# Performance work log

Hardware: AMD Instinct MI355X
Metric: run time of the kernel (lower is better)

## Reference

```python
import jax, jax.numpy as jnp
import numpy as np

VOCAB, EMB, HID, NCLS = 50257, 48, 128, 2000
B, S = 512, 1024


def setup_inputs() -> dict:
    key = jax.random.key(0)
    ks = jax.random.split(key, 8)
    x = jax.random.randint(ks[0], (B, S), 0, VOCAB)
    emb_table = jax.random.normal(ks[1], (VOCAB, EMB), dtype=jnp.float32)
    emb_table = emb_table.at[0].set(0.0)  # padding_idx=0
    k_ih = 1.0 / np.sqrt(HID)
    w_ih = jax.random.uniform(ks[2], (4 * HID, EMB), minval=-k_ih, maxval=k_ih, dtype=jnp.float32)
    w_hh = jax.random.uniform(ks[3], (4 * HID, HID), minval=-k_ih, maxval=k_ih, dtype=jnp.float32)
    b_ih = jax.random.uniform(ks[4], (4 * HID,), minval=-k_ih, maxval=k_ih, dtype=jnp.float32)
    b_hh = jax.random.uniform(ks[5], (4 * HID,), minval=-k_ih, maxval=k_ih, dtype=jnp.float32)
    k_fc = 1.0 / np.sqrt(HID)
    w_fc = jax.random.uniform(ks[6], (NCLS, HID), minval=-k_fc, maxval=k_fc, dtype=jnp.float32)
    b_fc = jax.random.uniform(ks[7], (NCLS,), minval=-k_fc, maxval=k_fc, dtype=jnp.float32)
    return {"x": x, "emb_table": emb_table, "w_ih": w_ih, "w_hh": w_hh,
            "b_ih": b_ih, "b_hh": b_hh, "w_fc": w_fc, "b_fc": b_fc}


def _lstm_last_hidden(e, w_ih, w_hh, b_ih, b_hh):
    # e: [B, S, E]. Precompute input contributions for all timesteps (one big GEMM).
    xg = jnp.einsum('bse,ge->bsg', e, w_ih) + b_ih + b_hh  # [B, S, 4H]
    xg = jnp.transpose(xg, (1, 0, 2))                      # [S, B, 4H]
    Bn = e.shape[0]
    h0 = jnp.zeros((Bn, HID), e.dtype)
    c0 = jnp.zeros((Bn, HID), e.dtype)

    def step(carry, xg_t):
        h, c = carry
        g = xg_t + h @ w_hh.T                              # [B, 4H]
        i, f, gg, o = jnp.split(g, 4, axis=-1)             # PyTorch gate order i,f,g,o
        i = jax.nn.sigmoid(i)
        f = jax.nn.sigmoid(f)
        gg = jnp.tanh(gg)
        o = jax.nn.sigmoid(o)
        c = f * c + i * gg
        h = o * jnp.tanh(c)
        return (h, c), None

    (h_n, _), _ = jax.lax.scan(step, (h0, c0), xg)
    return h_n


def reference(x, emb_table, w_ih, w_hh, b_ih, b_hh, w_fc, b_fc):
    e = emb_table[x]                                       # [B, S, E] gather
    h_n = _lstm_last_hidden(e, w_ih, w_hh, b_ih, b_hh)     # [B, H]
    return h_n @ w_fc.T + b_fc                             # [B, NCLS]
```

## Files before the change

### kernel.cpp

```cpp
#include <hip/hip_runtime.h>

#define DI __device__ __forceinline__

typedef unsigned int uint;
typedef unsigned short ushort;
typedef _Float16 half2t __attribute__((ext_vector_type(2)));

#define VOCAB 50257
#define NEMB 48
#define HID 128
#define G4 512
#define NCLS 2000
#define BATCH 512
#define SEQ 1024

#if __has_builtin(__builtin_amdgcn_fdot2)
DI float fdot2(half2t a, half2t b, float c) { return __builtin_amdgcn_fdot2(a, b, c, false); }
#else
DI float fdot2(half2t a, half2t b, float c) { return c + (float)a.x * (float)b.x + (float)a.y * (float)b.y; }
#endif

DI float sigm(float x) {
  return __builtin_amdgcn_rcpf(1.0f + __builtin_amdgcn_exp2f(-1.4426950408889634f * x));
}
DI float tanhfast(float x) {
  return 1.0f - 2.0f * __builtin_amdgcn_rcpf(__builtin_amdgcn_exp2f(2.8853900817779268f * x) + 1.0f);
}

DI void barrier_lds_only() {
  asm volatile("s_waitcnt lgkmcnt(0)" ::: "memory");
  __builtin_amdgcn_s_barrier();
  asm volatile("" ::: "memory");
}

#define VROWS 32
__global__ __launch_bounds__(512) void build_P(
    const float* __restrict__ emb, const float* __restrict__ w_ih,
    const float* __restrict__ b_ih, const float* __restrict__ b_hh,
    _Float16* __restrict__ P)
{
  __shared__ __align__(16) float eL[VROWS][NEMB];
  const int tid = threadIdx.x;
  const int v0 = blockIdx.x * VROWS;
  int nrows = VOCAB - v0; if (nrows > VROWS) nrows = VROWS;

  for (int f = tid; f < nrows * NEMB; f += 512)
    eL[f / NEMB][f % NEMB] = emb[(size_t)v0 * NEMB + f];

  float w[NEMB];
  {
    const float* wr = w_ih + (size_t)tid * NEMB;
#pragma unroll
    for (int k = 0; k < NEMB; k++) w[k] = wr[k];
  }
  float bias = b_ih[tid] + b_hh[tid];
  __syncthreads();

  for (int v = 0; v < nrows; v++) {
    const float4* e4 = (const float4*)&eL[v][0];
    float a = bias;
#pragma unroll
    for (int k = 0; k < NEMB / 4; k++) {
      float4 e = e4[k];
      a += w[4 * k] * e.x + w[4 * k + 1] * e.y + w[4 * k + 2] * e.z + w[4 * k + 3] * e.w;
    }
    P[(size_t)(v0 + v) * G4 + tid] = (_Float16)a;
  }
}

template<bool USE_P>
__global__ __launch_bounds__(512, 4) void lstm_scan(
    const int* __restrict__ x, const float* __restrict__ emb,
    const float* __restrict__ w_ih, const float* __restrict__ w_hh,
    const float* __restrict__ b_ih, const float* __restrict__ b_hh,
    const _Float16* __restrict__ P, float* __restrict__ hout)
{
  __shared__ int tokL[SEQ];
  __shared__ __align__(16) _Float16 h16[HID];
  __shared__ float g2h[2][G4];
  __shared__ __align__(8) half2t e16[2][NEMB / 2];

  const int tid = threadIdx.x;
  const int b = blockIdx.x;
  const int col = tid & 255;
  const int kh = tid >> 8;
  const int koff = kh * (HID / 2);

  {
    const int* xp = x + (size_t)b * SEQ;
#pragma unroll
    for (int i = 0; i < SEQ / 512; i++) tokL[tid + 512 * i] = xp[tid + 512 * i];
  }

  half2t w0[HID / 4], w1[HID / 4];
  {
    const float4* wr0 = (const float4*)(w_hh + (size_t)col * HID + koff);
    const float4* wr1 = (const float4*)(w_hh + (size_t)(col + 256) * HID + koff);
#pragma unroll
    for (int k = 0; k < HID / 8; k++) {
      float4 a = wr0[k];
      half2t p; p.x = (_Float16)a.x; p.y = (_Float16)a.y; w0[2 * k] = p;
      p.x = (_Float16)a.z; p.y = (_Float16)a.w; w0[2 * k + 1] = p;
      float4 bv = wr1[k];
      p.x = (_Float16)bv.x; p.y = (_Float16)bv.y; w1[2 * k] = p;
      p.x = (_Float16)bv.z; p.y = (_Float16)bv.w; w1[2 * k + 1] = p;
    }
  }
  half2t wih0[NEMB / 2], wih1[NEMB / 2];
  float bias0 = 0.0f, bias1 = 0.0f;
  if (!USE_P && kh == 0) {
    const float* wr0 = w_ih + (size_t)col * NEMB;
    const float* wr1 = w_ih + (size_t)(col + 256) * NEMB;
#pragma unroll
    for (int k = 0; k < NEMB / 2; k++) {
      half2t p;
      p.x = (_Float16)wr0[2 * k]; p.y = (_Float16)wr0[2 * k + 1]; wih0[k] = p;
      p.x = (_Float16)wr1[2 * k]; p.y = (_Float16)wr1[2 * k + 1]; wih1[k] = p;
    }
    bias0 = b_ih[col] + b_hh[col];
    bias1 = b_ih[col + 256] + b_hh[col + 256];
  }
  if (tid < HID) h16[tid] = (_Float16)0.0f;
  __syncthreads();

  float c = 0.0f;
  _Float16 pa0{}, pa1{}, pb0{}, pb1{};
  float2 einfl = {0.0f, 0.0f};
  if (USE_P) {
    if (kh == 0) {
      const _Float16* r0 = P + (size_t)tokL[0] * G4;
      const _Float16* r1 = P + (size_t)tokL[1] * G4;
      pa0 = r0[col]; pa1 = r0[col + 256];
      pb0 = r1[col]; pb1 = r1[col + 256];
    }
  } else {
    if (tid < NEMB / 2) {
      float2 e0 = ((const float2*)(emb + (size_t)tokL[0] * NEMB))[tid];
      einfl    = ((const float2*)(emb + (size_t)tokL[1] * NEMB))[tid];
      half2t p; p.x = (_Float16)e0.x; p.y = (_Float16)e0.y;
      e16[0][tid] = p;
    }
  }
  __syncthreads();

#define STEP(t, par) do {                                                      \
    float xg0, xg1;                                                            \
    if (USE_P) {                                                               \
      if (kh == 0) {                                                           \
        int tc = (t) + 2; if (tc > SEQ - 1) tc = SEQ - 1;                      \
        xg0 = (float)((par) ? pb0 : pa0);                                      \
        xg1 = (float)((par) ? pb1 : pa1);                                      \
        const _Float16* rn = P + (size_t)tokL[tc] * G4;      \
        _Float16 n0 = rn[col], n1 = rn[col + 256];                             \
        if ((par) == 0) { pa0 = n0; pa1 = n1; } else { pb0 = n0; pb1 = n1; }   \
      } else { xg0 = 0.0f; xg1 = 0.0f; }                                       \
    } else {                                                                   \
      if (tid < NEMB / 2) {                                                    \
        int tc = (t) + 2; if (tc > SEQ - 1) tc = SEQ - 1;                      \
        half2t p; p.x = (_Float16)einfl.x; p.y = (_Float16)einfl.y;            \
        e16[((t) + 1) & 1][tid] = p;                                           \
        einfl = ((const float2*)(emb + (size_t)tokL[tc] * NEMB))[tid];         \
      }                                                                        \
      if (kh == 0) {                                                           \
        xg0 = bias0; xg1 = bias1;                                              \
        _Pragma("unroll")                                                      \
        for (int k = 0; k < NEMB / 2; k++) {                                   \
          xg0 = fdot2(wih0[k], e16[(par)][k], xg0);                            \
          xg1 = fdot2(wih1[k], e16[(par)][k], xg1);                            \
        }                                                                      \
      } else { xg0 = 0.0f; xg1 = 0.0f; }                                       \
    }                                                                          \
    const uint4* hv = (const uint4*)h16 + (kh << 3);                           \
    float s0 = xg0, u0 = 0.0f, s1 = xg1, u1 = 0.0f;                            \
    _Pragma("unroll")                                                          \
    for (int kt = 0; kt < HID / 16; kt++) {                                    \
      uint4 hq = hv[kt];                                                       \
      half2t ha = __builtin_bit_cast(half2t, hq.x);                            \
      half2t hb = __builtin_bit_cast(half2t, hq.y);                            \
      half2t hc = __builtin_bit_cast(half2t, hq.z);                            \
      half2t hd = __builtin_bit_cast(half2t, hq.w);                            \
      s0 = fdot2(w0[4 * kt + 0], ha, s0);                                      \
      u0 = fdot2(w0[4 * kt + 1], hb, u0);                                      \
      s0 = fdot2(w0[4 * kt + 2], hc, s0);                                      \
      u0 = fdot2(w0[4 * kt + 3], hd, u0);                                      \
      s1 = fdot2(w1[4 * kt + 0], ha, s1);                                      \
      u1 = fdot2(w1[4 * kt + 1], hb, u1);                                      \
      s1 = fdot2(w1[4 * kt + 2], hc, s1);                                      \
      u1 = fdot2(w1[4 * kt + 3], hd, u1);                                      \
    }                                                                          \
    g2h[kh][col] = s0 + u0;                                                    \
    g2h[kh][col + 256] = s1 + u1;                                              \
    barrier_lds_only();                                                        \
    if (tid < HID) {                                                           \
      float gi = g2h[0][tid]           + g2h[1][tid];                          \
      float gf = g2h[0][HID + tid]     + g2h[1][HID + tid];                    \
      float gc = g2h[0][2 * HID + tid] + g2h[1][2 * HID + tid];                \
      float go = g2h[0][3 * HID + tid] + g2h[1][3 * HID + tid];                \
      float fi = sigm(gi), ff = sigm(gf), gt = tanhfast(gc), fo = sigm(go);    \
      c = ff * c + fi * gt;                                                    \
      float hh = fo * tanhfast(c);                                             \
      h16[tid] = (_Float16)hh;                                                 \
      if ((t) == SEQ - 1) hout[(size_t)b * HID + tid] = hh;                    \
    }                                                                          \
    barrier_lds_only();                                                        \
  } while (0)

  for (int t = 0; t < SEQ; t += 2) { STEP(t, 0); STEP(t + 1, 1); }
#undef STEP
}

#define FCR 64
#define FCC 64
__global__ __launch_bounds__(256) void fc_kernel(
    const float* __restrict__ h, const float* __restrict__ w_fc,
    const float* __restrict__ b_fc, float* __restrict__ out)
{
  __shared__ float aT[HID][FCR];
  __shared__ float bT[HID][FCC];
  const int tid = threadIdx.x;
  const int r0 = blockIdx.y * FCR;
  const int c0 = blockIdx.x * FCC;

  for (int f = tid; f < FCR * (HID / 4); f += 256) {
    int row = f >> 5, q = f & 31;
    float4 v = ((const float4*)h)[(((size_t)(r0 + row)) << 5) + q];
    aT[4 * q + 0][row] = v.x; aT[4 * q + 1][row] = v.y;
    aT[4 * q + 2][row] = v.z; aT[4 * q + 3][row] = v.w;
    int wrow = c0 + row;
    float4 wv;
    if (wrow < NCLS) wv = ((const float4*)w_fc)[(((size_t)wrow) << 5) + q];
    else { wv.x = 0.f; wv.y = 0.f; wv.z = 0.f; wv.w = 0.f; }
    bT[4 * q + 0][row] = wv.x; bT[4 * q + 1][row] = wv.y;
    bT[4 * q + 2][row] = wv.z; bT[4 * q + 3][row] = wv.w;
  }
  __syncthreads();

  const int cr = tid & 15, rr = tid >> 4;
  float acc[4][4];
#pragma unroll
  for (int i = 0; i < 4; i++)
#pragma unroll
    for (int j = 0; j < 4; j++) acc[i][j] = 0.0f;

#pragma unroll 4
  for (int k = 0; k < HID; k++) {
    float4 av = *(const float4*)&aT[k][4 * rr];
    float4 bv = *(const float4*)&bT[k][4 * cr];
    float a[4] = {av.x, av.y, av.z, av.w};
    float bb[4] = {bv.x, bv.y, bv.z, bv.w};
#pragma unroll
    for (int i = 0; i < 4; i++)
#pragma unroll
      for (int j = 0; j < 4; j++) acc[i][j] += a[i] * bb[j];
  }

#pragma unroll
  for (int j = 0; j < 4; j++) {
    int cc = c0 + 4 * cr + j;
    if (cc < NCLS) {
      float bias = b_fc[cc];
#pragma unroll
      for (int i = 0; i < 4; i++)
        out[(size_t)(r0 + 4 * rr + i) * NCLS + cc] = acc[i][j] + bias;
    }
  }
}

extern "C" void kernel_launch(void* const* d_in, const int* in_sizes, int n_in,
                              void* d_out, int out_size, void* d_ws, size_t ws_size,
                              hipStream_t stream) {
  const int*   xx   = (const int*)d_in[0];
  const float* emb  = (const float*)d_in[1];
  const float* w_ih = (const float*)d_in[2];
  const float* w_hh = (const float*)d_in[3];
  const float* b_ih = (const float*)d_in[4];
  const float* b_hh = (const float*)d_in[5];
  const float* w_fc = (const float*)d_in[6];
  const float* b_fc = (const float*)d_in[7];
  float* out = (float*)d_out;

  const size_t pbytes = (size_t)VOCAB * G4 * sizeof(_Float16);
  const size_t palign = (pbytes + 255) & ~(size_t)255;
  const size_t hbytes = (size_t)BATCH * HID * sizeof(float);

  float* hout;
  if (ws_size >= palign + hbytes) {
    _Float16* P = (_Float16*)d_ws;
    hout = (float*)((char*)d_ws + palign);
    build_P<<<(VOCAB + VROWS - 1) / VROWS, 512, 0, stream>>>(emb, w_ih, b_ih, b_hh, P);
    lstm_scan<true><<<BATCH, 512, 0, stream>>>(xx, emb, w_ih, w_hh, b_ih, b_hh, P, hout);
  } else {
    hout = (float*)d_ws;
    lstm_scan<false><<<BATCH, 512, 0, stream>>>(xx, emb, w_ih, w_hh, b_ih, b_hh,
                                                (const _Float16*)nullptr, hout);
  }
  dim3 fcg((NCLS + FCC - 1) / FCC, BATCH / FCR);
  fc_kernel<<<fcg, 256, 0, stream>>>(hout, w_fc, b_fc, out);
}
```

Measured before the change: 1.004 ms.

## Drop second per-step barrier via per-wave redundant gate compute and private h

Every wave now computes the LSTM cell update for the 64 hidden units its own half of the recurrent dot product needs. Each wave writes those values into a wave-private h buffer, so the next step reads h without waiting for other waves. The gate-partial buffer is double-buffered by step parity, so the second barrier per timestep can be removed. In exchange, all 512 threads evaluate the transcendental gate math, where previously only 128 did, and the shared-memory footprint grows slightly.

```diff
diff --git a/kernel.cpp b/kernel.cpp
--- a/kernel.cpp
+++ b/kernel.cpp
@@ -76,15 +76,18 @@
     const _Float16* __restrict__ P, float* __restrict__ hout)
 {
   __shared__ int tokL[SEQ];
-  __shared__ __align__(16) _Float16 h16[HID];
-  __shared__ float g2h[2][G4];
+  __shared__ __align__(16) _Float16 hpriv[8][64];
+  __shared__ float g2[2][2][G4];
   __shared__ __align__(8) half2t e16[2][NEMB / 2];
 
   const int tid = threadIdx.x;
   const int b = blockIdx.x;
+  const int lane = tid & 63;
+  const int wave = tid >> 6;
   const int col = tid & 255;
   const int kh = tid >> 8;
   const int koff = kh * (HID / 2);
+  const int oidx = koff + lane;
 
   {
     const int* xp = x + (size_t)b * SEQ;
@@ -120,7 +123,7 @@
     bias0 = b_ih[col] + b_hh[col];
     bias1 = b_ih[col + 256] + b_hh[col + 256];
   }
-  if (tid < HID) h16[tid] = (_Float16)0.0f;
+  ((_Float16*)hpriv)[tid] = (_Float16)0.0f;
   __syncthreads();
 
   float c = 0.0f;
@@ -170,7 +173,8 @@
         }                                                                      \
       } else { xg0 = 0.0f; xg1 = 0.0f; }                                       \
     }                                                                          \
-    const uint4* hv = (const uint4*)h16 + (kh << 3);                           \
+        \
+    const uint4* hv = (const uint4*)&hpriv[wave][0];                           \
     float s0 = xg0, u0 = 0.0f, s1 = xg1, u1 = 0.0f;                            \
     _Pragma("unroll")                                                          \
     for (int kt = 0; kt < HID / 16; kt++) {                                    \
@@ -188,21 +192,23 @@
       s1 = fdot2(w1[4 * kt + 2], hc, s1);                                      \
       u1 = fdot2(w1[4 * kt + 3], hd, u1);                                      \
     }                                                                          \
-    g2h[kh][col] = s0 + u0;                                                    \
-    g2h[kh][col + 256] = s1 + u1;                                              \
+    g2[par][kh][col] = s0 + u0;                                                \
+    g2[par][kh][col + 256] = s1 + u1;                                          \
     barrier_lds_only();                                                        \
-    if (tid < HID) {                                                           \
-      float gi = g2h[0][tid]           + g2h[1][tid];                          \
-      float gf = g2h[0][HID + tid]     + g2h[1][HID + tid];                    \
-      float gc = g2h[0][2 * HID + tid] + g2h[1][2 * HID + tid];                \
-      float go = g2h[0][3 * HID + tid] + g2h[1][3 * HID + tid];                \
+         \
+    {                                                                          \
+      const float* gp = &g2[par][0][0];                                        \
+      float gi = gp[oidx]           + gp[G4 + oidx];                           \
+      float gf = gp[HID + oidx]     + gp[G4 + HID + oidx];                     \
+      float gc = gp[2 * HID + oidx] + gp[G4 + 2 * HID + oidx];                 \
+      float go = gp[3 * HID + oidx] + gp[G4 + 3 * HID + oidx];                 \
       float fi = sigm(gi), ff = sigm(gf), gt = tanhfast(gc), fo = sigm(go);    \
       c = ff * c + fi * gt;                                                    \
       float hh = fo * tanhfast(c);                                             \
-      h16[tid] = (_Float16)hh;                                                 \
-      if ((t) == SEQ - 1) hout[(size_t)b * HID + tid] = hh;                    \
+      hpriv[wave][lane] = (_Float16)hh;                                        \
+      if ((t) == SEQ - 1 && col < 64)                                          \
+        hout[(size_t)b * HID + oidx] = hh;                                     \
     }                                                                          \
-    barrier_lds_only();                                                        \
   } while (0)
 
   for (int t = 0; t < SEQ; t += 2) { STEP(t, 0); STEP(t + 1, 1); }
```

New measurement: 1.122 ms. +11.8%, slower.

## Batch 16 sequences per block and compute recurrent GEMM with MFMA

Applied to the files above, without the earlier changes.

Replaces the per-sequence LSTM scan (one block per batch row, fdot2 on VALU) with a kernel in which each block handles 16 sequences and computes h@W_hh^T with 16x16x32 f16 MFMA instructions, keeping W_hh fragments in registers. The precomputed input-projection table P is stored gate-interleaved so that each lane fetches its four gates with one 8-byte load, and h is double-buffered in swizzled LDS so only one barrier is needed per step. Only 32 blocks are launched, so the GPU is heavily underused, but each step does 16x more work per barrier. Token ids are narrowed to ushort in LDS.

```diff
diff --git a/kernel.cpp b/kernel.cpp
--- a/kernel.cpp
+++ b/kernel.cpp
@@ -5,6 +5,8 @@
 typedef unsigned int uint;
 typedef unsigned short ushort;
 typedef _Float16 half2t __attribute__((ext_vector_type(2)));
+typedef _Float16 f16x8 __attribute__((ext_vector_type(8)));
+typedef float f32x4 __attribute__((ext_vector_type(4)));
 
 #define VOCAB 50257
 #define NEMB 48
@@ -13,6 +15,8 @@
 #define NCLS 2000
 #define BATCH 512
 #define SEQ 1024
+#define MTILE 16
+#define NBLK (BATCH / MTILE)
 
 #if __has_builtin(__builtin_amdgcn_fdot2)
 DI float fdot2(half2t a, half2t b, float c) { return __builtin_amdgcn_fdot2(a, b, c, false); }
@@ -54,6 +58,7 @@
     for (int k = 0; k < NEMB; k++) w[k] = wr[k];
   }
   float bias = b_ih[tid] + b_hh[tid];
+  const int pidx = ((tid & 127) << 2) + (tid >> 7);
   __syncthreads();
 
   for (int v = 0; v < nrows; v++) {
@@ -64,16 +69,143 @@
       float4 e = e4[k];
       a += w[4 * k] * e.x + w[4 * k + 1] * e.y + w[4 * k + 2] * e.z + w[4 * k + 3] * e.w;
     }
-    P[(size_t)(v0 + v) * G4 + tid] = (_Float16)a;
-  }
-}
-
-template<bool USE_P>
-__global__ __launch_bounds__(512, 4) void lstm_scan(
+    P[(size_t)(v0 + v) * G4 + pidx] = (_Float16)a;
+  }
+}
+
+__global__ __launch_bounds__(512, 2) void lstm_mfma(
+    const int* __restrict__ x, const float* __restrict__ w_hh,
+    const _Float16* __restrict__ P, float* __restrict__ hout)
+{
+  __shared__ ushort tokL[MTILE * SEQ];
+  __shared__ __align__(16) _Float16 hbuf[2][MTILE * HID];
+
+  const int tid  = threadIdx.x;
+  const int lane = tid & 63;
+  const int wave = tid >> 6;
+  const int l15  = lane & 15;
+  const int lg   = lane >> 4;
+  const int u    = wave * 16 + l15;
+  const int blk  = blockIdx.x;
+
+  {
+    const int* xp = x + (size_t)blk * MTILE * SEQ;
+    for (int i = tid; i < MTILE * SEQ; i += 512) tokL[i] = (ushort)xp[i];
+  }
+  {
+    uint4 z; z.x = z.y = z.z = z.w = 0u;
+    ((uint4*)&hbuf[0][0])[tid] = z;
+  }
+
+  f16x8 Bf[4][4];
+#pragma unroll
+  for (int n = 0; n < 4; n++) {
+    const float* wr = w_hh + (size_t)(n * 128 + u) * HID + lg * 8;
+#pragma unroll
+    for (int ck = 0; ck < 4; ck++) {
+      const float4* p4 = (const float4*)(wr + ck * 32);
+      float4 wa = p4[0], wb = p4[1];
+      f16x8 f;
+      f[0] = (_Float16)wa.x; f[1] = (_Float16)wa.y;
+      f[2] = (_Float16)wa.z; f[3] = (_Float16)wa.w;
+      f[4] = (_Float16)wb.x; f[5] = (_Float16)wb.y;
+      f[6] = (_Float16)wb.z; f[7] = (_Float16)wb.w;
+      Bf[n][ck] = f;
+    }
+  }
+
+  int aoff[4], woff[4], toff4[4];
+#pragma unroll
+  for (int ck = 0; ck < 4; ck++)
+    aoff[ck] = l15 * 256 + (((ck * 4 + lg) ^ l15) << 4);
+  const int gW = u >> 3;
+#pragma unroll
+  for (int r = 0; r < 4; r++) {
+    int row = lg * 4 + r;
+    woff[r]  = row * 256 + ((gW ^ row) << 4) + (u & 7) * 2;
+    toff4[r] = row * SEQ;
+  }
+
+  __syncthreads();
+
+  float cst[4] = {0.f, 0.f, 0.f, 0.f};
+
+  uint2 xgA[4], xgB[4];
+#pragma unroll
+  for (int r = 0; r < 4; r++) {
+    int t0 = tokL[toff4[r] + 0];
+    int t1 = tokL[toff4[r] + 1];
+    xgA[r] = *(const uint2*)(P + (size_t)t0 * G4 + u * 4);
+    xgB[r] = *(const uint2*)(P + (size_t)t1 * G4 + u * 4);
+  }
+
+#define STEP(t, par) do {                                                      \
+                 \
+    f32x4 ac0, ac1, ac2, ac3;                                                  \
+    _Pragma("unroll")                                                          \
+    for (int r = 0; r < 4; r++) {                                              \
+      uint2 v = (par) ? xgB[r] : xgA[r];                                       \
+      half2t p0 = __builtin_bit_cast(half2t, v.x);                             \
+      half2t p1 = __builtin_bit_cast(half2t, v.y);                             \
+      ac0[r] = (float)p0.x; ac1[r] = (float)p0.y;                              \
+      ac2[r] = (float)p1.x; ac3[r] = (float)p1.y;                              \
+    }                                                                          \
+              \
+    {                                                                          \
+      int tc = (t) + 2; if (tc > SEQ - 1) tc = SEQ - 1;                        \
+      _Pragma("unroll")                                                        \
+      for (int r = 0; r < 4; r++) {                                            \
+        int tk = tokL[toff4[r] + tc];                                          \
+        uint2 v = *(const uint2*)(P + (size_t)tk * G4 + u * 4);                \
+        if (par) xgB[r] = v; else xgA[r] = v;                                  \
+      }                                                                        \
+    }                                                                          \
+          \
+    const char* hc = (const char*)&hbuf[(t) & 1][0];                           \
+    f16x8 A0 = *(const f16x8*)(hc + aoff[0]);                                  \
+    f16x8 A1 = *(const f16x8*)(hc + aoff[1]);                                  \
+    f16x8 A2 = *(const f16x8*)(hc + aoff[2]);                                  \
+    f16x8 A3 = *(const f16x8*)(hc + aoff[3]);                                  \
+    ac0 = __builtin_amdgcn_mfma_f32_16x16x32_f16(A0, Bf[0][0], ac0, 0, 0, 0);  \
+    ac1 = __builtin_amdgcn_mfma_f32_16x16x32_f16(A0, Bf[1][0], ac1, 0, 0, 0);  \
+    ac2 = __builtin_amdgcn_mfma_f32_16x16x32_f16(A0, Bf[2][0], ac2, 0, 0, 0);  \
+    ac3 = __builtin_amdgcn_mfma_f32_16x16x32_f16(A0, Bf[3][0], ac3, 0, 0, 0);  \
+    ac0 = __builtin_amdgcn_mfma_f32_16x16x32_f16(A1, Bf[0][1], ac0, 0, 0, 0);  \
+    ac1 = __builtin_amdgcn_mfma_f32_16x16x32_f16(A1, Bf[1][1], ac1, 0, 0, 0);  \
+    ac2 = __builtin_amdgcn_mfma_f32_16x16x32_f16(A1, Bf[2][1], ac2, 0, 0, 0);  \
+    ac3 = __builtin_amdgcn_mfma_f32_16x16x32_f16(A1, Bf[3][1], ac3, 0, 0, 0);  \
+    ac0 = __builtin_amdgcn_mfma_f32_16x16x32_f16(A2, Bf[0][2], ac0, 0, 0, 0);  \
+    ac1 = __builtin_amdgcn_mfma_f32_16x16x32_f16(A2, Bf[1][2], ac1, 0, 0, 0);  \
+    ac2 = __builtin_amdgcn_mfma_f32_16x16x32_f16(A2, Bf[2][2], ac2, 0, 0, 0);  \
+    ac3 = __builtin_amdgcn_mfma_f32_16x16x32_f16(A2, Bf[3][2], ac3, 0, 0, 0);  \
+    ac0 = __builtin_amdgcn_mfma_f32_16x16x32_f16(A3, Bf[0][3], ac0, 0, 0, 0);  \
+    ac1 = __builtin_amdgcn_mfma_f32_16x16x32_f16(A3, Bf[1][3], ac1, 0, 0, 0);  \
+    ac2 = __builtin_amdgcn_mfma_f32_16x16x32_f16(A3, Bf[2][3], ac2, 0, 0, 0);  \
+    ac3 = __builtin_amdgcn_mfma_f32_16x16x32_f16(A3, Bf[3][3], ac3, 0, 0, 0);  \
+                \
+    char* hn = (char*)&hbuf[((t) + 1) & 1][0];                                 \
+    _Pragma("unroll")                                                          \
+    for (int r = 0; r < 4; r++) {                                              \
+      float iv = sigm(ac0[r]), fv = sigm(ac1[r]);                              \
+      float gv = tanhfast(ac2[r]), ov = sigm(ac3[r]);                          \
+      cst[r] = fv * cst[r] + iv * gv;                                          \
+      float hh = ov * tanhfast(cst[r]);                                        \
+      *(_Float16*)(hn + woff[r]) = (_Float16)hh;                               \
+      if ((t) == SEQ - 1)                                                      \
+        hout[((size_t)blk * MTILE + lg * 4 + r) * HID + u] = hh;               \
+    }                                                                          \
+    barrier_lds_only();                                                        \
+  } while (0)
+
+  for (int t = 0; t < SEQ; t += 2) { STEP(t, 0); STEP(t + 1, 1); }
+#undef STEP
+}
+
+__global__ __launch_bounds__(512, 4) void lstm_scan_fb(
     const int* __restrict__ x, const float* __restrict__ emb,
     const float* __restrict__ w_ih, const float* __restrict__ w_hh,
     const float* __restrict__ b_ih, const float* __restrict__ b_hh,
-    const _Float16* __restrict__ P, float* __restrict__ hout)
+    float* __restrict__ hout)
 {
   __shared__ int tokL[SEQ];
   __shared__ __align__(16) _Float16 h16[HID];
@@ -108,7 +240,7 @@
   }
   half2t wih0[NEMB / 2], wih1[NEMB / 2];
   float bias0 = 0.0f, bias1 = 0.0f;
-  if (!USE_P && kh == 0) {
+  if (kh == 0) {
     const float* wr0 = w_ih + (size_t)col * NEMB;
     const float* wr1 = w_ih + (size_t)(col + 256) * NEMB;
 #pragma unroll
@@ -124,52 +256,31 @@
   __syncthreads();
 
   float c = 0.0f;
-  _Float16 pa0{}, pa1{}, pb0{}, pb1{};
   float2 einfl = {0.0f, 0.0f};
-  if (USE_P) {
-    if (kh == 0) {
-      const _Float16* r0 = P + (size_t)tokL[0] * G4;
-      const _Float16* r1 = P + (size_t)tokL[1] * G4;
-      pa0 = r0[col]; pa1 = r0[col + 256];
-      pb0 = r1[col]; pb1 = r1[col + 256];
-    }
-  } else {
-    if (tid < NEMB / 2) {
-      float2 e0 = ((const float2*)(emb + (size_t)tokL[0] * NEMB))[tid];
-      einfl    = ((const float2*)(emb + (size_t)tokL[1] * NEMB))[tid];
-      half2t p; p.x = (_Float16)e0.x; p.y = (_Float16)e0.y;
-      e16[0][tid] = p;
-    }
+  if (tid < NEMB / 2) {
+    float2 e0 = ((const float2*)(emb + (size_t)tokL[0] * NEMB))[tid];
+    einfl    = ((const float2*)(emb + (size_t)tokL[1] * NEMB))[tid];
+    half2t p; p.x = (_Float16)e0.x; p.y = (_Float16)e0.y;
+    e16[0][tid] = p;
   }
   __syncthreads();
 
-#define STEP(t, par) do {                                                      \
+#define STEPF(t, par) do {                                                     \
     float xg0, xg1;                                                            \
-    if (USE_P) {                                                               \
-      if (kh == 0) {                                                           \
-        int tc = (t) + 2; if (tc > SEQ - 1) tc = SEQ - 1;                      \
-        xg0 = (float)((par) ? pb0 : pa0);                                      \
-        xg1 = (float)((par) ? pb1 : pa1);                                      \
-        const _Float16* rn = P + (size_t)tokL[tc] * G4;      \
-        _Float16 n0 = rn[col], n1 = rn[col + 256];                             \
-        if ((par) == 0) { pa0 = n0; pa1 = n1; } else { pb0 = n0; pb1 = n1; }   \
-      } else { xg0 = 0.0f; xg1 = 0.0f; }                                       \
-    } else {                                                                   \
-      if (tid < NEMB / 2) {                                                    \
-        int tc = (t) + 2; if (tc > SEQ - 1) tc = SEQ - 1;                      \
-        half2t p; p.x = (_Float16)einfl.x; p.y = (_Float16)einfl.y;            \
-        e16[((t) + 1) & 1][tid] = p;                                           \
-        einfl = ((const float2*)(emb + (size_t)tokL[tc] * NEMB))[tid];         \
+    if (tid < NEMB / 2) {                                                      \
+      int tc = (t) + 2; if (tc > SEQ - 1) tc = SEQ - 1;                        \
+      half2t p; p.x = (_Float16)einfl.x; p.y = (_Float16)einfl.y;              \
+      e16[((t) + 1) & 1][tid] = p;                                             \
+      einfl = ((const float2*)(emb + (size_t)tokL[tc] * NEMB))[tid];           \
+    }                                                                          \
+    if (kh == 0) {                                                             \
+      xg0 = bias0; xg1 = bias1;                                                \
+      _Pragma("unroll")                                                        \
+      for (int k = 0; k < NEMB / 2; k++) {                                     \
+        xg0 = fdot2(wih0[k], e16[(par)][k], xg0);                              \
+        xg1 = fdot2(wih1[k], e16[(par)][k], xg1);                              \
       }                                                                        \
-      if (kh == 0) {                                                           \
-        xg0 = bias0; xg1 = bias1;                                              \
-        _Pragma("unroll")                                                      \
-        for (int k = 0; k < NEMB / 2; k++) {                                   \
-          xg0 = fdot2(wih0[k], e16[(par)][k], xg0);                            \
-          xg1 = fdot2(wih1[k], e16[(par)][k], xg1);                            \
-        }                                                                      \
-      } else { xg0 = 0.0f; xg1 = 0.0f; }                                       \
-    }                                                                          \
+    } else { xg0 = 0.0f; xg1 = 0.0f; }                                         \
     const uint4* hv = (const uint4*)h16 + (kh << 3);                           \
     float s0 = xg0, u0 = 0.0f, s1 = xg1, u1 = 0.0f;                            \
     _Pragma("unroll")                                                          \
@@ -205,8 +316,8 @@
     barrier_lds_only();                                                        \
   } while (0)
 
-  for (int t = 0; t < SEQ; t += 2) { STEP(t, 0); STEP(t + 1, 1); }
-#undef STEP
+  for (int t = 0; t < SEQ; t += 2) { STEPF(t, 0); STEPF(t + 1, 1); }
+#undef STEPF
 }
 
 #define FCR 64
@@ -288,11 +399,10 @@
     _Float16* P = (_Float16*)d_ws;
     hout = (float*)((char*)d_ws + palign);
     build_P<<<(VOCAB + VROWS - 1) / VROWS, 512, 0, stream>>>(emb, w_ih, b_ih, b_hh, P);
-    lstm_scan<true><<<BATCH, 512, 0, stream>>>(xx, emb, w_ih, w_hh, b_ih, b_hh, P, hout);
+    lstm_mfma<<<NBLK, 512, 0, stream>>>(xx, w_hh, P, hout);
   } else {
     hout = (float*)d_ws;
-    lstm_scan<false><<<BATCH, 512, 0, stream>>>(xx, emb, w_ih, w_hh, b_ih, b_hh,
-                                                (const _Float16*)nullptr, hout);
+    lstm_scan_fb<<<BATCH, 512, 0, stream>>>(xx, emb, w_ih, w_hh, b_ih, b_hh, hout);
   }
   dim3 fcg((NCLS + FCC - 1) / FCC, BATCH / FCR);
   fc_kernel<<<fcg, 256, 0, stream>>>(hout, w_fc, b_fc, out);
```

After: 1.067 ms. 1.06x slower.
